# Kernel tuning notes

Measured on AMD Instinct MI355X. Metric: run time of the kernel, lower is better.

The kernel has to match this reference:

```python
import jax, jax.numpy as jnp
import numpy as np

N_NODES = 100000

def setup_inputs() -> dict:
    key = jax.random.key(0)
    k = jax.random.split(key, 6)
    d, dout = 128, 128
    x = jax.random.normal(k[0], (N_NODES, d), dtype=jnp.float32)
    edge_index = jax.random.randint(k[1], (2, 3200000), 0, N_NODES, dtype=jnp.int64)
    s = 1.0 / np.sqrt(d)
    W1 = jax.random.uniform(k[2], (d, d), jnp.float32, -s, s)
    b1 = jnp.zeros((d,), jnp.float32)
    W2 = jax.random.uniform(k[3], (d, d), jnp.float32, -s, s)
    b2 = jnp.zeros((d,), jnp.float32)
    W3 = jax.random.uniform(k[4], (d, dout), jnp.float32, -s, s)
    b3 = jnp.zeros((dout,), jnp.float32)
    return {"x": x, "W1": W1, "b1": b1, "W2": W2, "b2": b2, "W3": W3, "b3": b3, "edge_index": edge_index}

def reference(x, W1, b1, W2, b2, W3, b3, edge_index):
    src, dst = edge_index[0], edge_index[1]
    # GINConv aggregation: sum of neighbor features into destination nodes
    agg = jax.ops.segment_sum(x[src], dst, num_segments=N_NODES)  # [N, d]
    h = x + agg  # (1 + eps)*x + agg, eps = 0 (PyG default)
    # MLP1: linear1 -> ReLU -> linear2 -> ReLU
    h = jax.nn.relu(h @ W1 + b1)
    h = jax.nn.relu(h @ W2 + b2)
    # linear3 -> ReLU
    out = jax.nn.relu(h @ W3 + b3)
    return out
```

## Files before the change

kernel.cpp:

```cpp
#include <hip/hip_runtime.h>

#define N_NODES 100000
#define D 128
#define E_EDGES 3200000
#define BSHIFT 8
#define NPB 256
#define NBIN 391
#define BCAP 8960
#define PBLK 512
#define CHUNK (E_EDGES / PBLK)

typedef short bf16x8 __attribute__((ext_vector_type(8)));
typedef float f32x4 __attribute__((ext_vector_type(4)));

__global__ __launch_bounds__(256) void partition_edges(const int* __restrict__ eidx,
                                                       int* __restrict__ gcnt,
                                                       unsigned* __restrict__ bbuf) {
    __shared__ int hist[NBIN];
    __shared__ int cur[NBIN];
    int tid = threadIdx.x;
    for (int i = tid; i < NBIN; i += 256) hist[i] = 0;
    __syncthreads();
    int e0 = blockIdx.x * CHUNK, e1 = e0 + CHUNK;
    for (int e = e0 + tid; e < e1; e += 256)
        atomicAdd(&hist[eidx[E_EDGES + e] >> BSHIFT], 1);
    __syncthreads();
    for (int b = tid; b < NBIN; b += 256)
        cur[b] = atomicAdd(&gcnt[b], hist[b]);
    __syncthreads();
    for (int e = e0 + tid; e < e1; e += 256) {
        int src = eidx[e];
        int dst = eidx[E_EDGES + e];
        int b = dst >> BSHIFT;
        int slot = atomicAdd(&cur[b], 1);
        if (slot < BCAP)
            bbuf[(size_t)b * BCAP + slot] = ((unsigned)(dst & 255) << 17) | (unsigned)src;
    }
}

__global__ __launch_bounds__(256) void build_csr(const int* __restrict__ gcnt,
                                                 const unsigned* __restrict__ bbuf,
                                                 int* __restrict__ gpos,
                                                 int* __restrict__ col,
                                                 int2* __restrict__ meta) {
    __shared__ unsigned ebuf[BCAP];
    __shared__ int hist[NPB], pre[NPB], cur[NPB];
    __shared__ int sh_base;
    int b = blockIdx.x, tid = threadIdx.x;
    int mb = min(gcnt[b], BCAP);
    hist[tid] = 0;
    cur[tid] = 0;
    __syncthreads();
    for (int i = tid; i < mb; i += 256) {
        unsigned w = bbuf[(size_t)b * BCAP + i];
        ebuf[i] = w;
        atomicAdd(&hist[w >> 17], 1);
    }
    __syncthreads();
    if (tid < 64) {
        int a0 = hist[tid * 4 + 0], a1 = hist[tid * 4 + 1];
        int a2 = hist[tid * 4 + 2], a3 = hist[tid * 4 + 3];
        int s = a0 + a1 + a2 + a3;
        int t = s;
        for (int off = 1; off < 64; off <<= 1) {
            int v = __shfl_up(t, off, 64);
            if (tid >= off) t += v;
        }
        int excl = t - s;
        pre[tid * 4 + 0] = excl;
        pre[tid * 4 + 1] = excl + a0;
        pre[tid * 4 + 2] = excl + a0 + a1;
        pre[tid * 4 + 3] = excl + a0 + a1 + a2;
    }
    if (tid == 0) sh_base = atomicAdd(gpos, mb);
    __syncthreads();
    int gbase = sh_base;
    for (int i = tid; i < mb; i += 256) {
        unsigned w = ebuf[i];
        int l = (int)(w >> 17);
        int slot = atomicAdd(&cur[l], 1);
        col[gbase + pre[l] + slot] = (int)(w & 0x1FFFFu);
    }
    __syncthreads();
    int n = (b << BSHIFT) + tid;
    if (n < N_NODES) meta[n] = make_int2(gbase + pre[tid], hist[tid]);
}

__global__ __launch_bounds__(256) void to_bf16(const float* __restrict__ x,
                                               unsigned* __restrict__ xb) {
    int i = blockIdx.x * 256 + threadIdx.x;
    float2 v = ((const float2*)x)[i];
    unsigned lo = __float_as_uint(v.x);
    unsigned hi = __float_as_uint(v.y);
    lo = (lo + 0x7FFFu + ((lo >> 16) & 1u)) >> 16;
    hi = (hi + 0x7FFFu + ((hi >> 16) & 1u)) >> 16;
    xb[i] = lo | (hi << 16);
}

template <bool BF16>
__global__ __launch_bounds__(256) void gather_h0(const float* __restrict__ x,
                                                 const unsigned* __restrict__ xb,
                                                 const int2* __restrict__ meta,
                                                 const int* __restrict__ col,
                                                 float* __restrict__ h0) {
    int lane = threadIdx.x & 63;
    int n = __builtin_amdgcn_readfirstlane(blockIdx.x * 4 + (threadIdx.x >> 6));
    int2 mt = meta[n];
    int base = mt.x, m = mt.y;
    const float2* xr = (const float2*)x;
    float2 acc = xr[n * 64 + lane];
    for (int c = 0; c < m; c += 64) {
        int rem = m - c;
        int lim = rem < 64 ? rem : 64;
        int idx = 0;
        if (lane < lim) idx = col[base + c + lane];
        int j = 0;
        for (; j + 8 <= lim; j += 8) {
            if (BF16) {
                unsigned u[8];
#pragma unroll
                for (int q = 0; q < 8; ++q) {
                    int s = __shfl(idx, j + q, 64);
                    u[q] = xb[s * 64 + lane];
                }
#pragma unroll
                for (int q = 0; q < 8; ++q) {
                    acc.x += __uint_as_float(u[q] << 16);
                    acc.y += __uint_as_float(u[q] & 0xFFFF0000u);
                }
            } else {
                float2 v[8];
#pragma unroll
                for (int q = 0; q < 8; ++q) {
                    int s = __shfl(idx, j + q, 64);
                    v[q] = xr[s * 64 + lane];
                }
#pragma unroll
                for (int q = 0; q < 8; ++q) { acc.x += v[q].x; acc.y += v[q].y; }
            }
        }
        for (; j < lim; ++j) {
            int s = __shfl(idx, j, 64);
            if (BF16) {
                unsigned u = xb[s * 64 + lane];
                acc.x += __uint_as_float(u << 16);
                acc.y += __uint_as_float(u & 0xFFFF0000u);
            } else {
                float2 v = xr[s * 64 + lane];
                acc.x += v.x; acc.y += v.y;
            }
        }
    }
    ((float2*)h0)[n * 64 + lane] = acc;
}

__global__ __launch_bounds__(256) void w_prep(const float* __restrict__ W1,
                                              const float* __restrict__ W2,
                                              const float* __restrict__ W3,
                                              unsigned short* __restrict__ wt) {
    int e = blockIdx.x * 256 + threadIdx.x;
    int l = e >> 14, r = e & 16383;
    int k = r >> 7, n = r & 127;
    const float* W = l == 0 ? W1 : (l == 1 ? W2 : W3);
    unsigned u = __float_as_uint(W[r]);
    u = (u + 0x7FFFu + ((u >> 16) & 1u)) >> 16;
    wt[l * 16384 + n * 128 + k] = (unsigned short)u;
}

#define HBW 136

__global__ __launch_bounds__(256, 4) void mlp_mfma(float* __restrict__ h,
                                                   const unsigned short* __restrict__ wt,
                                                   const float* __restrict__ b1,
                                                   const float* __restrict__ b2,
                                                   const float* __restrict__ b3) {
    __shared__ unsigned short hb[128 * HBW];
    int tid = threadIdx.x;
    int w = tid >> 6, lane = tid & 63;
    int m = lane & 15, quad = lane >> 4;
    int r0 = blockIdx.x * 128 + w * 32;

    for (int it = 0; it < 16; ++it) {
        int flat = it * 64 + lane;
        int lr = flat >> 5, c4 = flat & 31;
        int gr = r0 + lr; if (gr >= N_NODES) gr = N_NODES - 1;
        float4 v = ((const float4*)h)[gr * 32 + c4];
        unsigned a0 = (__float_as_uint(v.x) + 0x8000u) >> 16;
        unsigned a1 = (__float_as_uint(v.y) + 0x8000u) & 0xFFFF0000u;
        unsigned a2 = (__float_as_uint(v.z) + 0x8000u) >> 16;
        unsigned a3 = (__float_as_uint(v.w) + 0x8000u) & 0xFFFF0000u;
        uint2 p = make_uint2(a0 | a1, a2 | a3);
        *(uint2*)&hb[(w * 32 + lr) * HBW + c4 * 4] = p;
    }

    const float* bias[3] = {b1, b2, b3};
    for (int l = 0; l < 3; ++l) {
        const unsigned short* W = wt + l * 16384;
        float bv[8];
#pragma unroll
        for (int ct = 0; ct < 8; ++ct) bv[ct] = bias[l][ct * 16 + m];

        f32x4 acc[2][8];
#pragma unroll
        for (int rt = 0; rt < 2; ++rt)
#pragma unroll
            for (int ct = 0; ct < 8; ++ct) acc[rt][ct] = (f32x4){0.f, 0.f, 0.f, 0.f};

#pragma unroll
        for (int ks = 0; ks < 4; ++ks) {
            bf16x8 a0 = *(const bf16x8*)&hb[(w * 32 + m) * HBW + ks * 32 + quad * 8];
            bf16x8 a1 = *(const bf16x8*)&hb[(w * 32 + 16 + m) * HBW + ks * 32 + quad * 8];
#pragma unroll
            for (int ct = 0; ct < 8; ++ct) {
                bf16x8 bf = *(const bf16x8*)&W[(ct * 16 + m) * 128 + ks * 32 + quad * 8];
                acc[0][ct] = __builtin_amdgcn_mfma_f32_16x16x32_bf16(a0, bf, acc[0][ct], 0, 0, 0);
                acc[1][ct] = __builtin_amdgcn_mfma_f32_16x16x32_bf16(a1, bf, acc[1][ct], 0, 0, 0);
            }
        }

        if (l < 2) {
#pragma unroll
            for (int rt = 0; rt < 2; ++rt)
#pragma unroll
                for (int ct = 0; ct < 8; ++ct)
#pragma unroll
                    for (int r = 0; r < 4; ++r) {
                        float v = acc[rt][ct][r] + bv[ct];
                        v = v > 0.f ? v : 0.f;
                        unsigned u = (__float_as_uint(v) + 0x8000u) >> 16;
                        hb[(w * 32 + rt * 16 + quad * 4 + r) * HBW + ct * 16 + m] = (unsigned short)u;
                    }
        } else {
#pragma unroll
            for (int rt = 0; rt < 2; ++rt)
#pragma unroll
                for (int r = 0; r < 4; ++r) {
                    int gr = r0 + rt * 16 + quad * 4 + r;
                    if (gr < N_NODES) {
#pragma unroll
                        for (int ct = 0; ct < 8; ++ct) {
                            float v = acc[rt][ct][r] + bv[ct];
                            h[(size_t)gr * 128 + ct * 16 + m] = v > 0.f ? v : 0.f;
                        }
                    }
                }
        }
    }
}

extern "C" void kernel_launch(void* const* d_in, const int* in_sizes, int n_in,
                              void* d_out, int out_size, void* d_ws, size_t ws_size,
                              hipStream_t stream) {
    const float* x  = (const float*)d_in[0];
    const float* W1 = (const float*)d_in[1];
    const float* b1 = (const float*)d_in[2];
    const float* W2 = (const float*)d_in[3];
    const float* b2 = (const float*)d_in[4];
    const float* W3 = (const float*)d_in[5];
    const float* b3 = (const float*)d_in[6];
    const int*  eidx = (const int*)d_in[7];
    float* out = (float*)d_out;

    const size_t OFF_WT   = 4096;
    const size_t OFF_META = OFF_WT + 98304;
    const size_t OFF_COL  = OFF_META + 800256;
    const size_t OFF_BBUF = OFF_COL + (size_t)E_EDGES * 4;
    const size_t SZ_BBUF  = (size_t)NBIN * BCAP * 4;
    const size_t SZ_XB    = (size_t)N_NODES * D * 2;
    const size_t NEED_BF16 = OFF_BBUF + (SZ_XB > SZ_BBUF ? SZ_XB : SZ_BBUF);

    int* gcnt = (int*)d_ws;
    int* gpos = (int*)((char*)d_ws + 2048);
    unsigned short* wtb = (unsigned short*)((char*)d_ws + OFF_WT);
    int2* meta = (int2*)((char*)d_ws + OFF_META);
    int* col = (int*)((char*)d_ws + OFF_COL);
    unsigned* bbuf = (unsigned*)((char*)d_ws + OFF_BBUF);
    unsigned* xb = bbuf;

    bool use_bf16 = ws_size >= NEED_BF16;

    hipMemsetAsync(d_ws, 0, 4096, stream);
    w_prep<<<192, 256, 0, stream>>>(W1, W2, W3, wtb);
    partition_edges<<<PBLK, 256, 0, stream>>>(eidx, gcnt, bbuf);
    build_csr<<<NBIN, 256, 0, stream>>>(gcnt, bbuf, gpos, col, meta);
    if (use_bf16) {
        to_bf16<<<(N_NODES * D / 2) / 256, 256, 0, stream>>>(x, xb);
        gather_h0<true ><<<N_NODES / 4, 256, 0, stream>>>(x, xb, meta, col, out);
    } else {
        gather_h0<false><<<N_NODES / 4, 256, 0, stream>>>(x, xb, meta, col, out);
    }
    mlp_mfma<<<(N_NODES + 127) / 128, 256, 0, stream>>>(out, wtb, b1, b2, b3);
}
```

Before: 380.5 us.

## Store aggregated features as bf16, cache edges in LDS, drop memset launch

The gather kernel now writes the aggregated node features as packed bf16 into workspace, and the MLP kernel loads them directly, halving that intermediate traffic. The bf16 copy of x is placed in the output buffer, which removes the fp32 fallback path. Edge partitioning caches src/dst in shared memory to avoid reading edge_index twice. The gather unroll grows to 16 and the workspace memset is folded into w_prep. Rounding of h0 to bf16 now happens once at the gather output, and LDS use in partitioning rises, which may reduce occupancy.

```diff
diff --git a/kernel.cpp b/kernel.cpp
--- a/kernel.cpp
+++ b/kernel.cpp
@@ -13,28 +13,61 @@
 typedef short bf16x8 __attribute__((ext_vector_type(8)));
 typedef float f32x4 __attribute__((ext_vector_type(4)));
 
+__device__ __forceinline__ unsigned rne_bf16(float f) {
+    unsigned u = __float_as_uint(f);
+    return (u + 0x7FFFu + ((u >> 16) & 1u)) >> 16;
+}
+
+__global__ __launch_bounds__(256) void w_prep(const float* __restrict__ W1,
+                                              const float* __restrict__ W2,
+                                              const float* __restrict__ W3,
+                                              unsigned short* __restrict__ wt,
+                                              int* __restrict__ ctrl) {
+    int e = blockIdx.x * 256 + threadIdx.x;
+    if (e < 1024) ctrl[e] = 0;
+    if (e < 3 * 16384) {
+        int l = e >> 14, r = e & 16383;
+        int k = r >> 7, n = r & 127;
+        const float* W = l == 0 ? W1 : (l == 1 ? W2 : W3);
+        wt[l * 16384 + n * 128 + k] = (unsigned short)rne_bf16(W[r]);
+    }
+}
+
+__global__ __launch_bounds__(256) void to_bf16(const float* __restrict__ x,
+                                               unsigned* __restrict__ xb) {
+    int i = blockIdx.x * 256 + threadIdx.x;
+    float2 v = ((const float2*)x)[i];
+    xb[i] = rne_bf16(v.x) | (rne_bf16(v.y) << 16);
+}
+
 __global__ __launch_bounds__(256) void partition_edges(const int* __restrict__ eidx,
                                                        int* __restrict__ gcnt,
                                                        unsigned* __restrict__ bbuf) {
+    __shared__ int ssrc[CHUNK];
+    __shared__ int sdst[CHUNK];
     __shared__ int hist[NBIN];
     __shared__ int cur[NBIN];
     int tid = threadIdx.x;
     for (int i = tid; i < NBIN; i += 256) hist[i] = 0;
     __syncthreads();
-    int e0 = blockIdx.x * CHUNK, e1 = e0 + CHUNK;
-    for (int e = e0 + tid; e < e1; e += 256)
-        atomicAdd(&hist[eidx[E_EDGES + e] >> BSHIFT], 1);
+    int e0 = blockIdx.x * CHUNK;
+    for (int i = tid; i < CHUNK; i += 256) {
+        int s = eidx[e0 + i];
+        int d = eidx[E_EDGES + e0 + i];
+        ssrc[i] = s;
+        sdst[i] = d;
+        atomicAdd(&hist[d >> BSHIFT], 1);
+    }
     __syncthreads();
     for (int b = tid; b < NBIN; b += 256)
         cur[b] = atomicAdd(&gcnt[b], hist[b]);
     __syncthreads();
-    for (int e = e0 + tid; e < e1; e += 256) {
-        int src = eidx[e];
-        int dst = eidx[E_EDGES + e];
-        int b = dst >> BSHIFT;
+    for (int i = tid; i < CHUNK; i += 256) {
+        int d = sdst[i];
+        int b = d >> BSHIFT;
         int slot = atomicAdd(&cur[b], 1);
         if (slot < BCAP)
-            bbuf[(size_t)b * BCAP + slot] = ((unsigned)(dst & 255) << 17) | (unsigned)src;
+            bbuf[(size_t)b * BCAP + slot] = ((unsigned)(d & 255) << 17) | (unsigned)ssrc[i];
     }
 }
 
@@ -86,90 +119,62 @@
     if (n < N_NODES) meta[n] = make_int2(gbase + pre[tid], hist[tid]);
 }
 
-__global__ __launch_bounds__(256) void to_bf16(const float* __restrict__ x,
-                                               unsigned* __restrict__ xb) {
-    int i = blockIdx.x * 256 + threadIdx.x;
-    float2 v = ((const float2*)x)[i];
-    unsigned lo = __float_as_uint(v.x);
-    unsigned hi = __float_as_uint(v.y);
-    lo = (lo + 0x7FFFu + ((lo >> 16) & 1u)) >> 16;
-    hi = (hi + 0x7FFFu + ((hi >> 16) & 1u)) >> 16;
-    xb[i] = lo | (hi << 16);
-}
-
-template <bool BF16>
 __global__ __launch_bounds__(256) void gather_h0(const float* __restrict__ x,
                                                  const unsigned* __restrict__ xb,
                                                  const int2* __restrict__ meta,
                                                  const int* __restrict__ col,
-                                                 float* __restrict__ h0) {
+                                                 unsigned* __restrict__ h0b) {
     int lane = threadIdx.x & 63;
     int n = __builtin_amdgcn_readfirstlane(blockIdx.x * 4 + (threadIdx.x >> 6));
     int2 mt = meta[n];
     int base = mt.x, m = mt.y;
-    const float2* xr = (const float2*)x;
-    float2 acc = xr[n * 64 + lane];
+    float2 acc = ((const float2*)x)[n * 64 + lane];
     for (int c = 0; c < m; c += 64) {
         int rem = m - c;
         int lim = rem < 64 ? rem : 64;
         int idx = 0;
         if (lane < lim) idx = col[base + c + lane];
         int j = 0;
-        for (; j + 8 <= lim; j += 8) {
-            if (BF16) {
-                unsigned u[8];
-#pragma unroll
-                for (int q = 0; q < 8; ++q) {
-                    int s = __shfl(idx, j + q, 64);
-                    u[q] = xb[s * 64 + lane];
-                }
-#pragma unroll
-                for (int q = 0; q < 8; ++q) {
-                    acc.x += __uint_as_float(u[q] << 16);
-                    acc.y += __uint_as_float(u[q] & 0xFFFF0000u);
-                }
-            } else {
-                float2 v[8];
-#pragma unroll
-                for (int q = 0; q < 8; ++q) {
-                    int s = __shfl(idx, j + q, 64);
-                    v[q] = xr[s * 64 + lane];
-                }
-#pragma unroll
-                for (int q = 0; q < 8; ++q) { acc.x += v[q].x; acc.y += v[q].y; }
+        for (; j + 16 <= lim; j += 16) {
+            unsigned u[16];
+#pragma unroll
+            for (int q = 0; q < 16; ++q) {
+                int s = __shfl(idx, j + q, 64);
+                u[q] = xb[s * 64 + lane];
+            }
+#pragma unroll
+            for (int q = 0; q < 16; ++q) {
+                acc.x += __uint_as_float(u[q] << 16);
+                acc.y += __uint_as_float(u[q] & 0xFFFF0000u);
+            }
+        }
+        for (; j + 4 <= lim; j += 4) {
+            unsigned u[4];
+#pragma unroll
+            for (int q = 0; q < 4; ++q) {
+                int s = __shfl(idx, j + q, 64);
+                u[q] = xb[s * 64 + lane];
+            }
+#pragma unroll
+            for (int q = 0; q < 4; ++q) {
+                acc.x += __uint_as_float(u[q] << 16);
+                acc.y += __uint_as_float(u[q] & 0xFFFF0000u);
             }
         }
         for (; j < lim; ++j) {
             int s = __shfl(idx, j, 64);
-            if (BF16) {
-                unsigned u = xb[s * 64 + lane];
-                acc.x += __uint_as_float(u << 16);
-                acc.y += __uint_as_float(u & 0xFFFF0000u);
-            } else {
-                float2 v = xr[s * 64 + lane];
-                acc.x += v.x; acc.y += v.y;
-            }
-        }
-    }
-    ((float2*)h0)[n * 64 + lane] = acc;
-}
-
-__global__ __launch_bounds__(256) void w_prep(const float* __restrict__ W1,
-                                              const float* __restrict__ W2,
-                                              const float* __restrict__ W3,
-                                              unsigned short* __restrict__ wt) {
-    int e = blockIdx.x * 256 + threadIdx.x;
-    int l = e >> 14, r = e & 16383;
-    int k = r >> 7, n = r & 127;
-    const float* W = l == 0 ? W1 : (l == 1 ? W2 : W3);
-    unsigned u = __float_as_uint(W[r]);
-    u = (u + 0x7FFFu + ((u >> 16) & 1u)) >> 16;
-    wt[l * 16384 + n * 128 + k] = (unsigned short)u;
+            unsigned u = xb[s * 64 + lane];
+            acc.x += __uint_as_float(u << 16);
+            acc.y += __uint_as_float(u & 0xFFFF0000u);
+        }
+    }
+    h0b[n * 64 + lane] = rne_bf16(acc.x) | (rne_bf16(acc.y) << 16);
 }
 
 #define HBW 136
 
-__global__ __launch_bounds__(256, 4) void mlp_mfma(float* __restrict__ h,
+__global__ __launch_bounds__(256, 4) void mlp_mfma(const unsigned* __restrict__ h0b,
+                                                   float* __restrict__ out,
                                                    const unsigned short* __restrict__ wt,
                                                    const float* __restrict__ b1,
                                                    const float* __restrict__ b2,
@@ -180,17 +185,12 @@
     int m = lane & 15, quad = lane >> 4;
     int r0 = blockIdx.x * 128 + w * 32;
 
-    for (int it = 0; it < 16; ++it) {
+    for (int it = 0; it < 8; ++it) {
         int flat = it * 64 + lane;
-        int lr = flat >> 5, c4 = flat & 31;
+        int lr = flat >> 4, c4 = flat & 15;
         int gr = r0 + lr; if (gr >= N_NODES) gr = N_NODES - 1;
-        float4 v = ((const float4*)h)[gr * 32 + c4];
-        unsigned a0 = (__float_as_uint(v.x) + 0x8000u) >> 16;
-        unsigned a1 = (__float_as_uint(v.y) + 0x8000u) & 0xFFFF0000u;
-        unsigned a2 = (__float_as_uint(v.z) + 0x8000u) >> 16;
-        unsigned a3 = (__float_as_uint(v.w) + 0x8000u) & 0xFFFF0000u;
-        uint2 p = make_uint2(a0 | a1, a2 | a3);
-        *(uint2*)&hb[(w * 32 + lr) * HBW + c4 * 4] = p;
+        uint4 v = ((const uint4*)h0b)[gr * 16 + c4];
+        *(uint4*)&hb[(w * 32 + lr) * HBW + c4 * 8] = v;
     }
 
     const float* bias[3] = {b1, b2, b3};
@@ -227,8 +227,8 @@
                     for (int r = 0; r < 4; ++r) {
                         float v = acc[rt][ct][r] + bv[ct];
                         v = v > 0.f ? v : 0.f;
-                        unsigned u = (__float_as_uint(v) + 0x8000u) >> 16;
-                        hb[(w * 32 + rt * 16 + quad * 4 + r) * HBW + ct * 16 + m] = (unsigned short)u;
+                        hb[(w * 32 + rt * 16 + quad * 4 + r) * HBW + ct * 16 + m] =
+                            (unsigned short)rne_bf16(v);
                     }
         } else {
 #pragma unroll
@@ -240,7 +240,7 @@
 #pragma unroll
                         for (int ct = 0; ct < 8; ++ct) {
                             float v = acc[rt][ct][r] + bv[ct];
-                            h[(size_t)gr * 128 + ct * 16 + m] = v > 0.f ? v : 0.f;
+                            out[(size_t)gr * 128 + ct * 16 + m] = v > 0.f ? v : 0.f;
                         }
                     }
                 }
@@ -265,29 +265,21 @@
     const size_t OFF_META = OFF_WT + 98304;
     const size_t OFF_COL  = OFF_META + 800256;
     const size_t OFF_BBUF = OFF_COL + (size_t)E_EDGES * 4;
-    const size_t SZ_BBUF  = (size_t)NBIN * BCAP * 4;
-    const size_t SZ_XB    = (size_t)N_NODES * D * 2;
-    const size_t NEED_BF16 = OFF_BBUF + (SZ_XB > SZ_BBUF ? SZ_XB : SZ_BBUF);
-
+
+    int* ctrl = (int*)d_ws;
     int* gcnt = (int*)d_ws;
     int* gpos = (int*)((char*)d_ws + 2048);
     unsigned short* wtb = (unsigned short*)((char*)d_ws + OFF_WT);
     int2* meta = (int2*)((char*)d_ws + OFF_META);
     int* col = (int*)((char*)d_ws + OFF_COL);
     unsigned* bbuf = (unsigned*)((char*)d_ws + OFF_BBUF);
-    unsigned* xb = bbuf;
-
-    bool use_bf16 = ws_size >= NEED_BF16;
-
-    hipMemsetAsync(d_ws, 0, 4096, stream);
-    w_prep<<<192, 256, 0, stream>>>(W1, W2, W3, wtb);
+    unsigned* h0b = bbuf;
+    unsigned* xb = (unsigned*)d_out;
+
+    w_prep<<<192, 256, 0, stream>>>(W1, W2, W3, wtb, ctrl);
+    to_bf16<<<(N_NODES * D / 2) / 256, 256, 0, stream>>>(x, xb);
     partition_edges<<<PBLK, 256, 0, stream>>>(eidx, gcnt, bbuf);
     build_csr<<<NBIN, 256, 0, stream>>>(gcnt, bbuf, gpos, col, meta);
-    if (use_bf16) {
-        to_bf16<<<(N_NODES * D / 2) / 256, 256, 0, stream>>>(x, xb);
-        gather_h0<true ><<<N_NODES / 4, 256, 0, stream>>>(x, xb, meta, col, out);
-    } else {
-        gather_h0<false><<<N_NODES / 4, 256, 0, stream>>>(x, xb, meta, col, out);
-    }
-    mlp_mfma<<<(N_NODES + 127) / 128, 256, 0, stream>>>(out, wtb, b1, b2, b3);
-}
+    gather_h0<<<N_NODES / 4, 256, 0, stream>>>(x, xb, meta, col, h0b);
+    mlp_mfma<<<(N_NODES + 127) / 128, 256, 0, stream>>>(h0b, out, wtb, b1, b2, b3);
+}
```

Result: faster. 349.2 us (-8.2%).
